# Optimization experiments

Hardware: AMD Instinct MI355X
Metric: run time of the kernel (lower is better)

The kernel has to match this reference:

```python
import jax, jax.numpy as jnp
import numpy as np
from jax.ops import segment_sum, segment_max

N_NODES = 100000
N_EDGES = 1600000
IN_CH = 128
HIDDEN = 128
OUT_CH = 64
HEADS1 = 8


def _lin_params(key, din, dout, scale):
    kw, kb = jax.random.split(key)
    W = jax.random.normal(kw, (din, dout), jnp.float32) * scale
    b = jax.random.normal(kb, (dout,), jnp.float32) * 0.01
    return W, b


def setup_inputs() -> dict:
    key = jax.random.key(0)
    ks = jax.random.split(key, 10)
    x = jax.random.normal(ks[0], (N_NODES, IN_CH), jnp.float32)
    edge_index = jax.random.randint(ks[1], (2, N_EDGES), 0, N_NODES, jnp.int32)
    s1 = 1.0 / np.sqrt(IN_CH)
    Wq1, bq1 = _lin_params(ks[2], IN_CH, HIDDEN, s1)
    Wk1, bk1 = _lin_params(ks[3], IN_CH, HIDDEN, s1)
    Wv1, bv1 = _lin_params(ks[4], IN_CH, HIDDEN, s1)
    Ws1, bs1 = _lin_params(ks[5], IN_CH, HIDDEN, s1)
    s2 = 1.0 / np.sqrt(HIDDEN)
    Wq2, bq2 = _lin_params(ks[6], HIDDEN, OUT_CH, s2)
    Wk2, bk2 = _lin_params(ks[7], HIDDEN, OUT_CH, s2)
    Wv2, bv2 = _lin_params(ks[8], HIDDEN, OUT_CH, s2)
    Ws2, bs2 = _lin_params(ks[9], HIDDEN, OUT_CH, s2)
    return dict(x=x, edge_index=edge_index,
                Wq1=Wq1, bq1=bq1, Wk1=Wk1, bk1=bk1, Wv1=Wv1, bv1=bv1, Ws1=Ws1, bs1=bs1,
                Wq2=Wq2, bq2=bq2, Wk2=Wk2, bk2=bk2, Wv2=Wv2, bv2=bv2, Ws2=Ws2, bs2=bs2)


def transformer_conv(x, src, dst, Wq, bq, Wk, bk, Wv, bv, Ws, bs, heads, concat):
    # x: [N, Din]; src/dst: [E]; per-head dim C = Dout_total // heads
    N = x.shape[0]
    C = Wq.shape[1] // heads
    q = (x @ Wq + bq).reshape(N, heads, C)
    k = (x @ Wk + bk).reshape(N, heads, C)
    v = (x @ Wv + bv).reshape(N, heads, C)
    # edge-wise gather + dot-product attention logits: [E, H]
    alpha = jnp.einsum('ehc,ehc->eh', q[dst], k[src]) / np.sqrt(C)
    # softmax over incoming edges of each dst node (stable via segment max)
    m = segment_max(alpha, dst, num_segments=N)  # [N, H]
    ex = jnp.exp(alpha - jax.lax.stop_gradient(m)[dst])
    denom = segment_sum(ex, dst, num_segments=N)  # [N, H]
    alpha_n = ex / denom[dst]  # [E, H]
    out = segment_sum(v[src] * alpha_n[:, :, None], dst, num_segments=N)  # [N, H, C]
    skip = x @ Ws + bs  # root weight (PyG root_weight=True)
    if concat:
        out = out.reshape(N, heads * C) + skip
    else:
        out = out.mean(axis=1) + skip
    return out


def reference(x, edge_index,
              Wq1, bq1, Wk1, bk1, Wv1, bv1, Ws1, bs1,
              Wq2, bq2, Wk2, bk2, Wv2, bv2, Ws2, bs2):
    src, dst = edge_index[0], edge_index[1]
    h = transformer_conv(x, src, dst, Wq1, bq1, Wk1, bk1, Wv1, bv1, Ws1, bs1,
                         heads=HEADS1, concat=True)
    h = jax.nn.relu(h)  # dropout is identity in eval mode
    out = transformer_conv(h, src, dst, Wq2, bq2, Wk2, bk2, Wv2, bv2, Ws2, bs2,
                           heads=1, concat=False)
    return out
```

## Files before the change

### kernel.cpp

```cpp
#include <hip/hip_runtime.h>
#include <math.h>

#define NN 100000
#define NPAD 100096
#define NE 1600000
#define NB 391
#define BKSH 8
#define EPB 6250
#define CSTAGE 5120
#define NDEG 64
#define DTOT (NDEG * NB)

typedef __attribute__((ext_vector_type(8))) short bf16x8;
typedef __attribute__((ext_vector_type(4))) float f32x4;

__device__ __forceinline__ unsigned short f2bf(float x) {
  unsigned int u = __float_as_uint(x);
  u += 0x7fffu + ((u >> 16) & 1u);
  return (unsigned short)(u >> 16);
}
__device__ __forceinline__ float bf2f(unsigned short b) {
  return __uint_as_float(((unsigned int)b) << 16);
}
__device__ __forceinline__ void unpack8(uint4 u, float* f) {
  f[0] = __uint_as_float(u.x << 16); f[1] = __uint_as_float(u.x & 0xffff0000u);
  f[2] = __uint_as_float(u.y << 16); f[3] = __uint_as_float(u.y & 0xffff0000u);
  f[4] = __uint_as_float(u.z << 16); f[5] = __uint_as_float(u.z & 0xffff0000u);
  f[6] = __uint_as_float(u.w << 16); f[7] = __uint_as_float(u.w & 0xffff0000u);
}
__device__ __forceinline__ void split8(const float* f, bf16x8& h8, bf16x8& l8) {
  union { bf16x8 v; unsigned short s[8]; } H, L;
  #pragma unroll
  for (int j = 0; j < 8; ++j) {
    const unsigned short hh = f2bf(f[j]);
    H.s[j] = hh;
    L.s[j] = f2bf(f[j] - bf2f(hh));
  }
  h8 = H.v; l8 = L.v;
}
__device__ __forceinline__ void gl_lds16(const void* g, void* lds) {
  __builtin_amdgcn_global_load_lds(
      (const __attribute__((address_space(1))) unsigned int*)g,
      (__attribute__((address_space(3))) unsigned int*)lds, 16, 0, 0);
}

#define PIPE_WAIT4  asm volatile("s_waitcnt vmcnt(4)\n\ts_barrier" ::: "memory")
#define PIPE_WAIT36 asm volatile("s_waitcnt vmcnt(36)\n\ts_barrier" ::: "memory")
#define PIPE_WAIT0  asm volatile("s_waitcnt vmcnt(0)\n\ts_barrier" ::: "memory")
#define PIPE_BAR    asm volatile("s_barrier" ::: "memory")
#define PIPE_FENCE  asm volatile("" ::: "memory")

__global__ __launch_bounds__(256)
void bktcnt_k(const int* __restrict__ dst, int* __restrict__ gcnt) {
  __shared__ int cnt[NB];
  for (int i = threadIdx.x; i < NB; i += 256) cnt[i] = 0;
  __syncthreads();
  const int e0 = blockIdx.x * EPB;
  for (int e = e0 + threadIdx.x; e < e0 + EPB; e += 256)
    atomicAdd(&cnt[dst[e] >> BKSH], 1);
  __syncthreads();
  for (int i = threadIdx.x; i < NB; i += 256)
    if (cnt[i]) atomicAdd(&gcnt[i], cnt[i]);
}

__global__ void bktscan_k(const int* __restrict__ gcnt, int* __restrict__ base,
                          int* __restrict__ cursor) {
  __shared__ int sh[512];
  const int t = threadIdx.x;
  const int v = (t < NB) ? gcnt[t] : 0;
  sh[t] = v;
  __syncthreads();
  #pragma unroll
  for (int off = 1; off < 512; off <<= 1) {
    int nv = (t >= off) ? sh[t - off] : 0;
    __syncthreads();
    sh[t] += nv;
    __syncthreads();
  }
  const int excl = sh[t] - v;
  if (t < NB) { base[t] = excl; cursor[t] = excl; }
  if (t == NB - 1) base[NB] = excl + v;
}

__global__ __launch_bounds__(256)
void bktscat_k(const int* __restrict__ src, const int* __restrict__ dst,
               int* __restrict__ cursor, unsigned int* __restrict__ pairs) {
  __shared__ int cnt[NB];
  __shared__ int bbase[NB];
  for (int i = threadIdx.x; i < NB; i += 256) cnt[i] = 0;
  __syncthreads();
  const int e0 = blockIdx.x * EPB;
  for (int e = e0 + threadIdx.x; e < e0 + EPB; e += 256)
    atomicAdd(&cnt[dst[e] >> BKSH], 1);
  __syncthreads();
  for (int i = threadIdx.x; i < NB; i += 256) {
    bbase[i] = cnt[i] ? atomicAdd(&cursor[i], cnt[i]) : 0;
    cnt[i] = 0;
  }
  __syncthreads();
  for (int e = e0 + threadIdx.x; e < e0 + EPB; e += 256) {
    const int d = dst[e];
    const int b = d >> BKSH;
    const int loc = atomicAdd(&cnt[b], 1);
    pairs[bbase[b] + loc] = ((unsigned)src[e] << BKSH) | (unsigned)(d & 255);
  }
}

__global__ __launch_bounds__(256)
void bktcsr_k(const unsigned int* __restrict__ pairs, const int* __restrict__ base,
              int* __restrict__ rowp, int* __restrict__ cidx) {
  __shared__ int cnt[256];
  __shared__ int sums[256];
  __shared__ int stage[CSTAGE];
  const int b = blockIdx.x, t = threadIdx.x;
  const int p0 = base[b], p1 = base[b + 1], bs = p1 - p0;
  const int n0 = b << BKSH;
  const int nloc = (NN - n0 < 256) ? (NN - n0) : 256;
  cnt[t] = 0;
  __syncthreads();
  for (int i = p0 + t; i < p1; i += 256)
    atomicAdd(&cnt[pairs[i] & 255], 1);
  __syncthreads();
  const int v = cnt[t];
  sums[t] = v;
  __syncthreads();
  #pragma unroll
  for (int off = 1; off < 256; off <<= 1) {
    int nv = (t >= off) ? sums[t - off] : 0;
    __syncthreads();
    sums[t] += nv;
    __syncthreads();
  }
  const int myexcl = sums[t] - v;
  if (t < nloc) rowp[n0 + t] = p0 + myexcl;
  if (b == 0 && t == 0) rowp[NN] = base[NB];
  __syncthreads();
  cnt[t] = myexcl;
  __syncthreads();
  if (bs <= CSTAGE) {
    for (int i = p0 + t; i < p1; i += 256) {
      const unsigned pk = pairs[i];
      const int loc = atomicAdd(&cnt[pk & 255], 1);
      stage[loc] = (int)(pk >> BKSH);
    }
    __syncthreads();
    for (int i = t; i < bs; i += 256) cidx[p0 + i] = stage[i];
  } else {
    for (int i = p0 + t; i < p1; i += 256) {
      const unsigned pk = pairs[i];
      const int loc = atomicAdd(&cnt[pk & 255], 1);
      cidx[p0 + loc] = (int)(pk >> BKSH);
    }
  }
}

__global__ __launch_bounds__(256)
void dcnt_k(const int* __restrict__ rowp, int* __restrict__ gdcnt) {
  __shared__ int h[NDEG];
  const int t = threadIdx.x, b = blockIdx.x;
  if (t < NDEG) h[t] = 0;
  __syncthreads();
  const int n = b * 256 + t;
  if (n < NN) {
    int d = rowp[n + 1] - rowp[n];
    if (d > NDEG - 1) d = NDEG - 1;
    atomicAdd(&h[d], 1);
  }
  __syncthreads();
  if (t < NDEG) gdcnt[t * NB + b] = h[t];
}

__global__ __launch_bounds__(1024)
void dscan2_k(int* __restrict__ g) {
  __shared__ int part[1024];
  const int t = threadIdx.x;
  constexpr int PER = (DTOT + 1023) / 1024;
  int vals[PER];
  const int base = t * PER;
  int sum = 0;
  #pragma unroll
  for (int i = 0; i < PER; ++i) {
    const int idx = base + i;
    const int v = (idx < DTOT) ? g[idx] : 0;
    vals[i] = sum;
    sum += v;
  }
  part[t] = sum;
  __syncthreads();
  #pragma unroll
  for (int off = 1; off < 1024; off <<= 1) {
    int nv = (t >= off) ? part[t - off] : 0;
    __syncthreads();
    part[t] += nv;
    __syncthreads();
  }
  const int excl = part[t] - sum;
  #pragma unroll
  for (int i = 0; i < PER; ++i) {
    const int idx = base + i;
    if (idx < DTOT) g[idx] = excl + vals[i];
  }
}

__global__ __launch_bounds__(256)
void dperm2_k(const int* __restrict__ rowp, const int* __restrict__ gdcnt,
              int* __restrict__ perm) {
  __shared__ int lcur[NDEG];
  const int t = threadIdx.x, b = blockIdx.x;
  if (t < NDEG) lcur[t] = 0;
  __syncthreads();
  const int n = b * 256 + t;
  if (n < NN) {
    int d = rowp[n + 1] - rowp[n];
    if (d > NDEG - 1) d = NDEG - 1;
    const int r = atomicAdd(&lcur[d], 1);
    perm[NN - 1 - (gdcnt[d * NB + b] + r)] = n;
  }
}

struct WConv { const float* src; unsigned short* hi; unsigned short* lo; int dout; };
struct WConv8 { WConv m[8]; };

__global__ void wconv_k(WConv8 a) {
  const WConv w = a.m[blockIdx.x];
  const int n = 128 * w.dout;
  for (int i = threadIdx.x; i < n; i += blockDim.x) {
    const int c = i >> 7, kk = i & 127;
    const float x = w.src[(size_t)kk * w.dout + c];
    const unsigned short h = f2bf(x);
    w.hi[i] = h;
    w.lo[i] = f2bf(x - bf2f(h));
  }
}

struct GMat { const unsigned short* wh; const unsigned short* wl;
              const float* bias; float* outf; unsigned short* outb; };
struct GArgs { GMat m[4]; };

template <int DOUT, bool PRESPLIT>
__global__ __launch_bounds__(256, 3)
void gemm4_mfma(const float* __restrict__ X,
                const unsigned short* __restrict__ Xh,
                const unsigned short* __restrict__ Xl,
                int nrows, GArgs ga) {
  constexpr int NCG = DOUT / 64;
  constexpr int NS = 4 * NCG * 2;
  __shared__ __align__(16) unsigned short Bs[2][8192];
  const int t = threadIdx.x;
  const int w = t >> 6, l = t & 63;
  const int lr = l & 15, lg = l >> 4;
  const int row0 = blockIdx.x * 128;

  float bias_r[4][NCG][4];
  #pragma unroll
  for (int m = 0; m < 4; ++m)
    #pragma unroll
    for (int cg = 0; cg < NCG; ++cg)
      #pragma unroll
      for (int nf = 0; nf < 4; ++nf)
        bias_r[m][cg][nf] = ga.m[m].bias[cg * 64 + nf * 16 + lr];

  bf16x8 ah[2][4], al[2][4];
  #pragma unroll
  for (int rf = 0; rf < 2; ++rf) {
    const int r = row0 + w * 32 + rf * 16 + lr;
    if constexpr (!PRESPLIT) {
      const bool ok = r < nrows;
      const float* xp = &X[(size_t)r * 128];
      #pragma unroll
      for (int ks = 0; ks < 4; ++ks) {
        float f[8];
        if (ok) {
          *(float4*)&f[0] = *(const float4*)&xp[ks * 32 + lg * 8];
          *(float4*)&f[4] = *(const float4*)&xp[ks * 32 + lg * 8 + 4];
        } else {
          #pragma unroll
          for (int j = 0; j < 8; ++j) f[j] = 0.f;
        }
        split8(f, ah[rf][ks], al[rf][ks]);
      }
    } else {
      #pragma unroll
      for (int ks = 0; ks < 4; ++ks) {
        ah[rf][ks] = *(const bf16x8*)&Xh[(size_t)r * 128 + ks * 32 + lg * 8];
        al[rf][ks] = *(const bf16x8*)&Xl[(size_t)r * 128 + ks * 32 + lg * 8];
      }
    }
  }
  PIPE_FENCE;

  auto stage = [&](int buf, int s) {
    const int m = s / (NCG * 2);
    const int rem = s - m * (NCG * 2);
    const int cg = rem >> 1, pl = rem & 1;
    const char* gb = (const char*)((pl ? ga.m[m].wl : ga.m[m].wh) + cg * 64 * 128);
    char* lb = (char*)&Bs[buf][0];
    #pragma unroll
    for (int i = 0; i < 4; ++i) {
      const int seg = (w * 4 + i) << 10;
      const int o = seg + l * 16;
      const int osw = o ^ (((o >> 8) & 7) << 4);
      gl_lds16(gb + osw, lb + seg);
    }
  };

  f32x4 acc[4][2];
  stage(0, 0);
  int cur = 0;
  const int sw = (lr & 7) << 4;
  #pragma unroll
  for (int s = 0; s < NS; ++s) {
    if (s + 1 < NS) stage(cur ^ 1, s + 1);
    if (s == NS - 1)                { PIPE_WAIT0; }
    else if (s >= 2 && !(s & 1))    { PIPE_WAIT36; }
    else                            { PIPE_WAIT4;  }
    const int m = s / (NCG * 2);
    const int rem = s - m * (NCG * 2);
    const int cg = rem >> 1, pl = rem & 1;
    const char* lbase = (const char*)&Bs[cur][0];
    if (pl == 0) {
      #pragma unroll
      for (int nf = 0; nf < 4; ++nf) {
        const char* lp = lbase + nf * 4096 + lr * 256;
        bf16x8 bq[4];
        #pragma unroll
        for (int ks = 0; ks < 4; ++ks)
          bq[ks] = *(const bf16x8*)(lp + (((ks * 64 + lg * 16) ^ sw)));
        f32x4 a0 = {0.f, 0.f, 0.f, 0.f}, a1 = a0;
        #pragma unroll
        for (int ks = 0; ks < 4; ++ks) {
          a0 = __builtin_amdgcn_mfma_f32_16x16x32_bf16(ah[0][ks], bq[ks], a0, 0, 0, 0);
          a1 = __builtin_amdgcn_mfma_f32_16x16x32_bf16(ah[1][ks], bq[ks], a1, 0, 0, 0);
        }
        #pragma unroll
        for (int ks = 0; ks < 4; ++ks) {
          a0 = __builtin_amdgcn_mfma_f32_16x16x32_bf16(al[0][ks], bq[ks], a0, 0, 0, 0);
          a1 = __builtin_amdgcn_mfma_f32_16x16x32_bf16(al[1][ks], bq[ks], a1, 0, 0, 0);
        }
        acc[nf][0] = a0; acc[nf][1] = a1;
      }
    } else {
      const GMat gm = ga.m[m];
      #pragma unroll
      for (int nf = 0; nf < 4; ++nf) {
        const char* lp = lbase + nf * 4096 + lr * 256;
        bf16x8 bq[4];
        #pragma unroll
        for (int ks = 0; ks < 4; ++ks)
          bq[ks] = *(const bf16x8*)(lp + (((ks * 64 + lg * 16) ^ sw)));
        f32x4 a0 = acc[nf][0], a1 = acc[nf][1];
        #pragma unroll
        for (int ks = 0; ks < 4; ++ks) {
          a0 = __builtin_amdgcn_mfma_f32_16x16x32_bf16(ah[0][ks], bq[ks], a0, 0, 0, 0);
          a1 = __builtin_amdgcn_mfma_f32_16x16x32_bf16(ah[1][ks], bq[ks], a1, 0, 0, 0);
        }
        const int col = cg * 64 + nf * 16 + lr;
        const float bb = bias_r[m][cg][nf];
        #pragma unroll
        for (int j = 0; j < 4; ++j) {
          const int r0 = row0 + w * 32 + lg * 4 + j;
          const int r1 = r0 + 16;
          if (gm.outb) {
            gm.outb[(size_t)r0 * DOUT + col] = f2bf(a0[j] + bb);
            gm.outb[(size_t)r1 * DOUT + col] = f2bf(a1[j] + bb);
          } else {
            gm.outf[(size_t)r0 * DOUT + col] = a0[j] + bb;
            gm.outf[(size_t)r1 * DOUT + col] = a1[j] + bb;
          }
        }
      }
    }
    if (s + 1 < NS) PIPE_BAR;
    cur ^= 1;
  }
}

__global__ __launch_bounds__(256)
void attn1_k(const unsigned short* __restrict__ q, const unsigned short* __restrict__ k,
             const unsigned short* __restrict__ v, const float* __restrict__ skip,
             const int* __restrict__ rowp, const int* __restrict__ cidx,
             const int* __restrict__ perm,
             unsigned short* __restrict__ hhi, unsigned short* __restrict__ hlo) {
  const int idx = blockIdx.x * 32 + (threadIdx.x >> 3);
  if (idx >= NN) return;
  const int node = perm[idx];
  const int cb = (threadIdx.x & 7) * 16;
  float qv[16];
  {
    uint4 q0 = *(const uint4*)&q[(size_t)node * 128 + cb];
    uint4 q1 = *(const uint4*)&q[(size_t)node * 128 + cb + 8];
    unpack8(q0, qv); unpack8(q1, qv + 8);
    #pragma unroll
    for (int c = 0; c < 16; ++c) qv[c] *= 0.25f;
  }
  float s = 0.f, acc[16];
  #pragma unroll
  for (int c = 0; c < 16; ++c) acc[c] = 0.f;
  const int e0 = rowp[node], e1 = rowp[node + 1];
  int e = e0;
  for (; e + 3 < e1; e += 4) {
    int sidx[4];
    #pragma unroll
    for (int j = 0; j < 4; ++j) sidx[j] = cidx[e + j];
    uint4 K[4][2], V[4][2];
    #pragma unroll
    for (int j = 0; j < 4; ++j) {
      const size_t o = (size_t)sidx[j] * 128 + cb;
      K[j][0] = *(const uint4*)&k[o];
      K[j][1] = *(const uint4*)&k[o + 8];
      V[j][0] = *(const uint4*)&v[o];
      V[j][1] = *(const uint4*)&v[o + 8];
    }
    float pr[4];
    #pragma unroll
    for (int j = 0; j < 4; ++j) {
      float kv[16];
      unpack8(K[j][0], kv); unpack8(K[j][1], kv + 8);
      float d = 0.f;
      #pragma unroll
      for (int c = 0; c < 16; ++c) d = fmaf(qv[c], kv[c], d);
      pr[j] = __expf(d);
      s += pr[j];
    }
    #pragma unroll
    for (int j = 0; j < 4; ++j) {
      float vv[16];
      unpack8(V[j][0], vv); unpack8(V[j][1], vv + 8);
      #pragma unroll
      for (int c = 0; c < 16; ++c) acc[c] = fmaf(pr[j], vv[c], acc[c]);
    }
  }
  for (; e < e1; ++e) {
    const int sa = cidx[e];
    uint4 k0 = *(const uint4*)&k[(size_t)sa * 128 + cb];
    uint4 k1 = *(const uint4*)&k[(size_t)sa * 128 + cb + 8];
    uint4 v0 = *(const uint4*)&v[(size_t)sa * 128 + cb];
    uint4 v1 = *(const uint4*)&v[(size_t)sa * 128 + cb + 8];
    float kv[16]; unpack8(k0, kv); unpack8(k1, kv + 8);
    float d = 0.f;
    #pragma unroll
    for (int c = 0; c < 16; ++c) d = fmaf(qv[c], kv[c], d);
    const float p = __expf(d);
    s += p;
    float vv[16]; unpack8(v0, vv); unpack8(v1, vv + 8);
    #pragma unroll
    for (int c = 0; c < 16; ++c) acc[c] = fmaf(p, vv[c], acc[c]);
  }
  const float inv = (e1 > e0) ? 1.f / s : 0.f;
  float sk[16];
  {
    const float* sp = &skip[(size_t)node * 128 + cb];
    *(float4*)&sk[0]  = *(const float4*)&sp[0];
    *(float4*)&sk[4]  = *(const float4*)&sp[4];
    *(float4*)&sk[8]  = *(const float4*)&sp[8];
    *(float4*)&sk[12] = *(const float4*)&sp[12];
  }
  unsigned int hw[8], lw[8];
  #pragma unroll
  for (int c2 = 0; c2 < 8; ++c2) {
    const float oa = fmaxf(fmaf(acc[2 * c2], inv, sk[2 * c2]), 0.f);
    const float ob = fmaxf(fmaf(acc[2 * c2 + 1], inv, sk[2 * c2 + 1]), 0.f);
    const unsigned short ha = f2bf(oa), hb = f2bf(ob);
    hw[c2] = (unsigned)ha | ((unsigned)hb << 16);
    lw[c2] = (unsigned)f2bf(oa - bf2f(ha)) | ((unsigned)f2bf(ob - bf2f(hb)) << 16);
  }
  uint4* HH = (uint4*)&hhi[(size_t)node * 128 + cb];
  uint4* LL = (uint4*)&hlo[(size_t)node * 128 + cb];
  HH[0] = make_uint4(hw[0], hw[1], hw[2], hw[3]);
  HH[1] = make_uint4(hw[4], hw[5], hw[6], hw[7]);
  LL[0] = make_uint4(lw[0], lw[1], lw[2], lw[3]);
  LL[1] = make_uint4(lw[4], lw[5], lw[6], lw[7]);
}

__global__ __launch_bounds__(256)
void attn2_k(const unsigned short* __restrict__ q, const unsigned short* __restrict__ k,
             const unsigned short* __restrict__ v, const float* __restrict__ skip,
             const int* __restrict__ rowp, const int* __restrict__ cidx,
             const int* __restrict__ perm, float* __restrict__ out) {
  const int idx = blockIdx.x * 32 + (threadIdx.x >> 3);
  if (idx >= NN) return;
  const int node = perm[idx];
  const int cb = (threadIdx.x & 7) * 8;
  float qv[8];
  {
    uint4 q0 = *(const uint4*)&q[(size_t)node * 64 + cb];
    unpack8(q0, qv);
    #pragma unroll
    for (int c = 0; c < 8; ++c) qv[c] *= 0.125f;
  }
  float s = 0.f, acc[8];
  #pragma unroll
  for (int c = 0; c < 8; ++c) acc[c] = 0.f;
  const int e0 = rowp[node], e1 = rowp[node + 1];
  int e = e0;
  for (; e + 3 < e1; e += 4) {
    int sidx[4];
    #pragma unroll
    for (int j = 0; j < 4; ++j) sidx[j] = cidx[e + j];
    uint4 K[4], V[4];
    #pragma unroll
    for (int j = 0; j < 4; ++j) {
      const size_t o = (size_t)sidx[j] * 64 + cb;
      K[j] = *(const uint4*)&k[o];
      V[j] = *(const uint4*)&v[o];
    }
    float dd[4];
    #pragma unroll
    for (int j = 0; j < 4; ++j) {
      float kv[8]; unpack8(K[j], kv);
      float d = 0.f;
      #pragma unroll
      for (int c = 0; c < 8; ++c) d = fmaf(qv[c], kv[c], d);
      dd[j] = d;
    }
    #pragma unroll
    for (int j = 0; j < 4; ++j) {
      dd[j] += __shfl_xor(dd[j], 1);
      dd[j] += __shfl_xor(dd[j], 2);
      dd[j] += __shfl_xor(dd[j], 4);
    }
    #pragma unroll
    for (int j = 0; j < 4; ++j) {
      const float p = __expf(dd[j]);
      s += p;
      float vv[8]; unpack8(V[j], vv);
      #pragma unroll
      for (int c = 0; c < 8; ++c) acc[c] = fmaf(p, vv[c], acc[c]);
    }
  }
  for (; e < e1; ++e) {
    const int sa = cidx[e];
    uint4 kk = *(const uint4*)&k[(size_t)sa * 64 + cb];
    uint4 vv4 = *(const uint4*)&v[(size_t)sa * 64 + cb];
    float kv[8]; unpack8(kk, kv);
    float d = 0.f;
    #pragma unroll
    for (int c = 0; c < 8; ++c) d = fmaf(qv[c], kv[c], d);
    d += __shfl_xor(d, 1);
    d += __shfl_xor(d, 2);
    d += __shfl_xor(d, 4);
    const float p = __expf(d);
    s += p;
    float vv[8]; unpack8(vv4, vv);
    #pragma unroll
    for (int c = 0; c < 8; ++c) acc[c] = fmaf(p, vv[c], acc[c]);
  }
  const float inv = (e1 > e0) ? 1.f / s : 0.f;
  const float* sp = &skip[(size_t)node * 64 + cb];
  float4 o0, o1;
  o0.x = fmaf(acc[0], inv, sp[0]); o0.y = fmaf(acc[1], inv, sp[1]);
  o0.z = fmaf(acc[2], inv, sp[2]); o0.w = fmaf(acc[3], inv, sp[3]);
  o1.x = fmaf(acc[4], inv, sp[4]); o1.y = fmaf(acc[5], inv, sp[5]);
  o1.z = fmaf(acc[6], inv, sp[6]); o1.w = fmaf(acc[7], inv, sp[7]);
  *(float4*)&out[(size_t)node * 64 + cb] = o0;
  *(float4*)&out[(size_t)node * 64 + cb + 4] = o1;
}

extern "C" void kernel_launch(void* const* d_in, const int* in_sizes, int n_in,
                              void* d_out, int out_size, void* d_ws, size_t ws_size,
                              hipStream_t stream) {
  const float* x = (const float*)d_in[0];
  const int* ei = (const int*)d_in[1];
  const int* esrc = ei;
  const int* edst = ei + NE;
  const float* Wf[8] = {(const float*)d_in[2],  (const float*)d_in[4],
                        (const float*)d_in[6],  (const float*)d_in[8],
                        (const float*)d_in[10], (const float*)d_in[12],
                        (const float*)d_in[14], (const float*)d_in[16]};
  const float* Bf[8] = {(const float*)d_in[3],  (const float*)d_in[5],
                        (const float*)d_in[7],  (const float*)d_in[9],
                        (const float*)d_in[11], (const float*)d_in[13],
                        (const float*)d_in[15], (const float*)d_in[17]};
  float* out = (float*)d_out;

  char* p = (char*)d_ws;
  auto alloc = [&](size_t b) { char* r = p; p += (b + 255) & ~(size_t)255; return r; };
  unsigned short* q1 = (unsigned short*)alloc((size_t)NPAD * 128 * 2);
  unsigned short* k1 = (unsigned short*)alloc((size_t)NPAD * 128 * 2);
  unsigned short* v1 = (unsigned short*)alloc((size_t)NPAD * 128 * 2);
  float*          sk1 = (float*)alloc((size_t)NPAD * 128 * 4);
  unsigned short* hh = (unsigned short*)alloc((size_t)NPAD * 128 * 2);
  unsigned short* hl = (unsigned short*)alloc((size_t)NPAD * 128 * 2);
  unsigned short* q2 = (unsigned short*)alloc((size_t)NPAD * 64 * 2);
  unsigned short* k2 = (unsigned short*)alloc((size_t)NPAD * 64 * 2);
  unsigned short* v2 = (unsigned short*)alloc((size_t)NPAD * 64 * 2);
  float*          sk2 = (float*)alloc((size_t)NPAD * 64 * 4);
  unsigned short* wh[8];
  unsigned short* wl[8];
  for (int i = 0; i < 8; ++i) {
    const int dout = (i < 4) ? 128 : 64;
    wh[i] = (unsigned short*)alloc((size_t)128 * dout * 2);
    wl[i] = (unsigned short*)alloc((size_t)128 * dout * 2);
  }
  int* rowp = (int*)alloc((size_t)(NN + 1) * 4);
  int* cidx = (int*)alloc((size_t)NE * 4);
  int* gcnt = (int*)alloc((size_t)NB * 4);
  int* base = (int*)alloc((size_t)(NB + 1) * 4);
  int* cursor = (int*)alloc((size_t)NB * 4);
  int* gdcnt = (int*)alloc((size_t)DTOT * 4);
  int* perm = (int*)alloc((size_t)NN * 4);
  unsigned int* pairs = (unsigned int*)hh;

  WConv8 wc;
  for (int i = 0; i < 8; ++i) wc.m[i] = {Wf[i], wh[i], wl[i], (i < 4) ? 128 : 64};
  wconv_k<<<8, 1024, 0, stream>>>(wc);

  hipMemsetAsync(gcnt, 0, NB * sizeof(int), stream);
  bktcnt_k<<<256, 256, 0, stream>>>(edst, gcnt);
  bktscan_k<<<1, 512, 0, stream>>>(gcnt, base, cursor);
  bktscat_k<<<256, 256, 0, stream>>>(esrc, edst, cursor, pairs);
  bktcsr_k<<<NB, 256, 0, stream>>>(pairs, base, rowp, cidx);

  dcnt_k<<<NB, 256, 0, stream>>>(rowp, gdcnt);
  dscan2_k<<<1, 1024, 0, stream>>>(gdcnt);
  dperm2_k<<<NB, 256, 0, stream>>>(rowp, gdcnt, perm);

  GArgs g1;
  g1.m[0] = {wh[0], wl[0], Bf[0], nullptr, q1};
  g1.m[1] = {wh[1], wl[1], Bf[1], nullptr, k1};
  g1.m[2] = {wh[2], wl[2], Bf[2], nullptr, v1};
  g1.m[3] = {wh[3], wl[3], Bf[3], sk1, nullptr};
  gemm4_mfma<128, false><<<NPAD / 128, 256, 0, stream>>>(x, nullptr, nullptr, NN, g1);
  attn1_k<<<(NN + 31) / 32, 256, 0, stream>>>(q1, k1, v1, sk1, rowp, cidx, perm, hh, hl);

  GArgs g2;
  g2.m[0] = {wh[4], wl[4], Bf[4], nullptr, q2};
  g2.m[1] = {wh[5], wl[5], Bf[5], nullptr, k2};
  g2.m[2] = {wh[6], wl[6], Bf[6], nullptr, v2};
  g2.m[3] = {wh[7], wl[7], Bf[7], sk2, nullptr};
  gemm4_mfma<64, true><<<NPAD / 128, 256, 0, stream>>>(nullptr, hh, hl, NN, g2);
  attn2_k<<<(NN + 31) / 32, 256, 0, stream>>>(q2, k2, v2, sk2, rowp, cidx, perm, out);
}
```

Baseline: 433.7 us.

## Split GEMM across two matrix groups, store skip in bf16, fuse degree histogram

The degree histogram moves into the CSR build kernel, which removes the separate dcnt launch and its rowp reread. The projection GEMM now uses a 2-D grid where each block computes two of the four matrices, with bias staged in shared memory. This frees registers, allowing occupancy 4, and doubles the block count. Skip outputs are stored as bf16 instead of fp32, halving that traffic, at some precision loss on the skip term. The cost is that every block now loads the X rows twice, once per grid-y slice.

Result: slower. 496.9 us (+14.6%).

```diff
diff --git a/kernel.cpp b/kernel.cpp
--- a/kernel.cpp
+++ b/kernel.cpp
@@ -108,21 +108,28 @@
 
 __global__ __launch_bounds__(256)
 void bktcsr_k(const unsigned int* __restrict__ pairs, const int* __restrict__ base,
-              int* __restrict__ rowp, int* __restrict__ cidx) {
+              int* __restrict__ rowp, int* __restrict__ cidx,
+              int* __restrict__ gdcnt) {
   __shared__ int cnt[256];
   __shared__ int sums[256];
+  __shared__ int hdeg[NDEG];
   __shared__ int stage[CSTAGE];
   const int b = blockIdx.x, t = threadIdx.x;
   const int p0 = base[b], p1 = base[b + 1], bs = p1 - p0;
   const int n0 = b << BKSH;
   const int nloc = (NN - n0 < 256) ? (NN - n0) : 256;
   cnt[t] = 0;
+  if (t < NDEG) hdeg[t] = 0;
   __syncthreads();
   for (int i = p0 + t; i < p1; i += 256)
     atomicAdd(&cnt[pairs[i] & 255], 1);
   __syncthreads();
   const int v = cnt[t];
   sums[t] = v;
+  if (t < nloc) {
+    int d = (v > NDEG - 1) ? NDEG - 1 : v;
+    atomicAdd(&hdeg[d], 1);
+  }
   __syncthreads();
   #pragma unroll
   for (int off = 1; off < 256; off <<= 1) {
@@ -134,6 +141,7 @@
   const int myexcl = sums[t] - v;
   if (t < nloc) rowp[n0 + t] = p0 + myexcl;
   if (b == 0 && t == 0) rowp[NN] = base[NB];
+  if (t < NDEG) gdcnt[t * NB + b] = hdeg[t];
   __syncthreads();
   cnt[t] = myexcl;
   __syncthreads();
@@ -152,22 +160,6 @@
       cidx[p0 + loc] = (int)(pk >> BKSH);
     }
   }
-}
-
-__global__ __launch_bounds__(256)
-void dcnt_k(const int* __restrict__ rowp, int* __restrict__ gdcnt) {
-  __shared__ int h[NDEG];
-  const int t = threadIdx.x, b = blockIdx.x;
-  if (t < NDEG) h[t] = 0;
-  __syncthreads();
-  const int n = b * 256 + t;
-  if (n < NN) {
-    int d = rowp[n + 1] - rowp[n];
-    if (d > NDEG - 1) d = NDEG - 1;
-    atomicAdd(&h[d], 1);
-  }
-  __syncthreads();
-  if (t < NDEG) gdcnt[t * NB + b] = h[t];
 }
 
 __global__ __launch_bounds__(1024)
@@ -234,31 +226,28 @@
 }
 
 struct GMat { const unsigned short* wh; const unsigned short* wl;
-              const float* bias; float* outf; unsigned short* outb; };
+              const float* bias; unsigned short* outb; };
 struct GArgs { GMat m[4]; };
 
 template <int DOUT, bool PRESPLIT>
-__global__ __launch_bounds__(256, 3)
+__global__ __launch_bounds__(256, 4)
 void gemm4_mfma(const float* __restrict__ X,
                 const unsigned short* __restrict__ Xh,
                 const unsigned short* __restrict__ Xl,
                 int nrows, GArgs ga) {
   constexpr int NCG = DOUT / 64;
-  constexpr int NS = 4 * NCG * 2;
+  constexpr int NS = 2 * NCG * 2;
   __shared__ __align__(16) unsigned short Bs[2][8192];
+  __shared__ float BiasS[2][DOUT];
+  const int mb = blockIdx.y * 2;
   const int t = threadIdx.x;
   const int w = t >> 6, l = t & 63;
   const int lr = l & 15, lg = l >> 4;
   const int row0 = blockIdx.x * 128;
 
-  float bias_r[4][NCG][4];
-  #pragma unroll
-  for (int m = 0; m < 4; ++m)
-    #pragma unroll
-    for (int cg = 0; cg < NCG; ++cg)
-      #pragma unroll
-      for (int nf = 0; nf < 4; ++nf)
-        bias_r[m][cg][nf] = ga.m[m].bias[cg * 64 + nf * 16 + lr];
+  for (int i = t; i < 2 * DOUT; i += 256)
+    BiasS[i / DOUT][i % DOUT] = ga.m[mb + i / DOUT].bias[i % DOUT];
+  __syncthreads();
 
   bf16x8 ah[2][4], al[2][4];
   #pragma unroll
@@ -290,10 +279,11 @@
   PIPE_FENCE;
 
   auto stage = [&](int buf, int s) {
-    const int m = s / (NCG * 2);
-    const int rem = s - m * (NCG * 2);
+    const int ml = s / (NCG * 2);
+    const int rem = s - ml * (NCG * 2);
     const int cg = rem >> 1, pl = rem & 1;
-    const char* gb = (const char*)((pl ? ga.m[m].wl : ga.m[m].wh) + cg * 64 * 128);
+    const GMat& gm = ga.m[mb + ml];
+    const char* gb = (const char*)((pl ? gm.wl : gm.wh) + cg * 64 * 128);
     char* lb = (char*)&Bs[buf][0];
     #pragma unroll
     for (int i = 0; i < 4; ++i) {
@@ -311,11 +301,11 @@
   #pragma unroll
   for (int s = 0; s < NS; ++s) {
     if (s + 1 < NS) stage(cur ^ 1, s + 1);
-    if (s == NS - 1)                { PIPE_WAIT0; }
-    else if (s >= 2 && !(s & 1))    { PIPE_WAIT36; }
-    else                            { PIPE_WAIT4;  }
-    const int m = s / (NCG * 2);
-    const int rem = s - m * (NCG * 2);
+    if (s == NS - 1)              { PIPE_WAIT0; }
+    else if (s >= 2 && !(s & 1))  { PIPE_WAIT36; }
+    else                          { PIPE_WAIT4;  }
+    const int ml = s / (NCG * 2);
+    const int rem = s - ml * (NCG * 2);
     const int cg = rem >> 1, pl = rem & 1;
     const char* lbase = (const char*)&Bs[cur][0];
     if (pl == 0) {
@@ -340,7 +330,7 @@
         acc[nf][0] = a0; acc[nf][1] = a1;
       }
     } else {
-      const GMat gm = ga.m[m];
+      const GMat gm = ga.m[mb + ml];
       #pragma unroll
       for (int nf = 0; nf < 4; ++nf) {
         const char* lp = lbase + nf * 4096 + lr * 256;
@@ -355,18 +345,13 @@
           a1 = __builtin_amdgcn_mfma_f32_16x16x32_bf16(ah[1][ks], bq[ks], a1, 0, 0, 0);
         }
         const int col = cg * 64 + nf * 16 + lr;
-        const float bb = bias_r[m][cg][nf];
+        const float bb = BiasS[ml][col];
         #pragma unroll
         for (int j = 0; j < 4; ++j) {
           const int r0 = row0 + w * 32 + lg * 4 + j;
           const int r1 = r0 + 16;
-          if (gm.outb) {
-            gm.outb[(size_t)r0 * DOUT + col] = f2bf(a0[j] + bb);
-            gm.outb[(size_t)r1 * DOUT + col] = f2bf(a1[j] + bb);
-          } else {
-            gm.outf[(size_t)r0 * DOUT + col] = a0[j] + bb;
-            gm.outf[(size_t)r1 * DOUT + col] = a1[j] + bb;
-          }
+          gm.outb[(size_t)r0 * DOUT + col] = f2bf(a0[j] + bb);
+          gm.outb[(size_t)r1 * DOUT + col] = f2bf(a1[j] + bb);
         }
       }
     }
@@ -377,7 +362,7 @@
 
 __global__ __launch_bounds__(256)
 void attn1_k(const unsigned short* __restrict__ q, const unsigned short* __restrict__ k,
-             const unsigned short* __restrict__ v, const float* __restrict__ skip,
+             const unsigned short* __restrict__ v, const unsigned short* __restrict__ skip,
              const int* __restrict__ rowp, const int* __restrict__ cidx,
              const int* __restrict__ perm,
              unsigned short* __restrict__ hhi, unsigned short* __restrict__ hlo) {
@@ -449,11 +434,10 @@
   const float inv = (e1 > e0) ? 1.f / s : 0.f;
   float sk[16];
   {
-    const float* sp = &skip[(size_t)node * 128 + cb];
-    *(float4*)&sk[0]  = *(const float4*)&sp[0];
-    *(float4*)&sk[4]  = *(const float4*)&sp[4];
-    *(float4*)&sk[8]  = *(const float4*)&sp[8];
-    *(float4*)&sk[12] = *(const float4*)&sp[12];
+    const unsigned short* sp = &skip[(size_t)node * 128 + cb];
+    uint4 s0v = *(const uint4*)&sp[0];
+    uint4 s1v = *(const uint4*)&sp[8];
+    unpack8(s0v, sk); unpack8(s1v, sk + 8);
   }
   unsigned int hw[8], lw[8];
   #pragma unroll
@@ -474,7 +458,7 @@
 
 __global__ __launch_bounds__(256)
 void attn2_k(const unsigned short* __restrict__ q, const unsigned short* __restrict__ k,
-             const unsigned short* __restrict__ v, const float* __restrict__ skip,
+             const unsigned short* __restrict__ v, const unsigned short* __restrict__ skip,
              const int* __restrict__ rowp, const int* __restrict__ cidx,
              const int* __restrict__ perm, float* __restrict__ out) {
   const int idx = blockIdx.x * 32 + (threadIdx.x >> 3);
@@ -546,12 +530,17 @@
     for (int c = 0; c < 8; ++c) acc[c] = fmaf(p, vv[c], acc[c]);
   }
   const float inv = (e1 > e0) ? 1.f / s : 0.f;
-  const float* sp = &skip[(size_t)node * 64 + cb];
+  float sk[8];
+  {
+    const unsigned short* sp = &skip[(size_t)node * 64 + cb];
+    uint4 sv = *(const uint4*)&sp[0];
+    unpack8(sv, sk);
+  }
   float4 o0, o1;
-  o0.x = fmaf(acc[0], inv, sp[0]); o0.y = fmaf(acc[1], inv, sp[1]);
-  o0.z = fmaf(acc[2], inv, sp[2]); o0.w = fmaf(acc[3], inv, sp[3]);
-  o1.x = fmaf(acc[4], inv, sp[4]); o1.y = fmaf(acc[5], inv, sp[5]);
-  o1.z = fmaf(acc[6], inv, sp[6]); o1.w = fmaf(acc[7], inv, sp[7]);
+  o0.x = fmaf(acc[0], inv, sk[0]); o0.y = fmaf(acc[1], inv, sk[1]);
+  o0.z = fmaf(acc[2], inv, sk[2]); o0.w = fmaf(acc[3], inv, sk[3]);
+  o1.x = fmaf(acc[4], inv, sk[4]); o1.y = fmaf(acc[5], inv, sk[5]);
+  o1.z = fmaf(acc[6], inv, sk[6]); o1.w = fmaf(acc[7], inv, sk[7]);
   *(float4*)&out[(size_t)node * 64 + cb] = o0;
   *(float4*)&out[(size_t)node * 64 + cb + 4] = o1;
 }
@@ -578,13 +567,13 @@
   unsigned short* q1 = (unsigned short*)alloc((size_t)NPAD * 128 * 2);
   unsigned short* k1 = (unsigned short*)alloc((size_t)NPAD * 128 * 2);
   unsigned short* v1 = (unsigned short*)alloc((size_t)NPAD * 128 * 2);
-  float*          sk1 = (float*)alloc((size_t)NPAD * 128 * 4);
+  unsigned short* sk1 = (unsigned short*)alloc((size_t)NPAD * 128 * 2);
   unsigned short* hh = (unsigned short*)alloc((size_t)NPAD * 128 * 2);
   unsigned short* hl = (unsigned short*)alloc((size_t)NPAD * 128 * 2);
   unsigned short* q2 = (unsigned short*)alloc((size_t)NPAD * 64 * 2);
   unsigned short* k2 = (unsigned short*)alloc((size_t)NPAD * 64 * 2);
   unsigned short* v2 = (unsigned short*)alloc((size_t)NPAD * 64 * 2);
-  float*          sk2 = (float*)alloc((size_t)NPAD * 64 * 4);
+  unsigned short* sk2 = (unsigned short*)alloc((size_t)NPAD * 64 * 2);
   unsigned short* wh[8];
   unsigned short* wl[8];
   for (int i = 0; i < 8; ++i) {
@@ -609,25 +598,26 @@
   bktcnt_k<<<256, 256, 0, stream>>>(edst, gcnt);
   bktscan_k<<<1, 512, 0, stream>>>(gcnt, base, cursor);
   bktscat_k<<<256, 256, 0, stream>>>(esrc, edst, cursor, pairs);
-  bktcsr_k<<<NB, 256, 0, stream>>>(pairs, base, rowp, cidx);
-
-  dcnt_k<<<NB, 256, 0, stream>>>(rowp, gdcnt);
+  bktcsr_k<<<NB, 256, 0, stream>>>(pairs, base, rowp, cidx, gdcnt);
+
   dscan2_k<<<1, 1024, 0, stream>>>(gdcnt);
   dperm2_k<<<NB, 256, 0, stream>>>(rowp, gdcnt, perm);
 
   GArgs g1;
-  g1.m[0] = {wh[0], wl[0], Bf[0], nullptr, q1};
-  g1.m[1] = {wh[1], wl[1], Bf[1], nullptr, k1};
-  g1.m[2] = {wh[2], wl[2], Bf[2], nullptr, v1};
-  g1.m[3] = {wh[3], wl[3], Bf[3], sk1, nullptr};
-  gemm4_mfma<128, false><<<NPAD / 128, 256, 0, stream>>>(x, nullptr, nullptr, NN, g1);
+  g1.m[0] = {wh[0], wl[0], Bf[0], q1};
+  g1.m[1] = {wh[1], wl[1], Bf[1], k1};
+  g1.m[2] = {wh[2], wl[2], Bf[2], v1};
+  g1.m[3] = {wh[3], wl[3], Bf[3], sk1};
+  gemm4_mfma<128, false><<<dim3(NPAD / 128, 2), 256, 0, stream>>>(
+      x, nullptr, nullptr, NN, g1);
   attn1_k<<<(NN + 31) / 32, 256, 0, stream>>>(q1, k1, v1, sk1, rowp, cidx, perm, hh, hl);
 
   GArgs g2;
-  g2.m[0] = {wh[4], wl[4], Bf[4], nullptr, q2};
-  g2.m[1] = {wh[5], wl[5], Bf[5], nullptr, k2};
-  g2.m[2] = {wh[6], wl[6], Bf[6], nullptr, v2};
-  g2.m[3] = {wh[7], wl[7], Bf[7], sk2, nullptr};
-  gemm4_mfma<64, true><<<NPAD / 128, 256, 0, stream>>>(nullptr, hh, hl, NN, g2);
+  g2.m[0] = {wh[4], wl[4], Bf[4], q2};
+  g2.m[1] = {wh[5], wl[5], Bf[5], k2};
+  g2.m[2] = {wh[6], wl[6], Bf[6], v2};
+  g2.m[3] = {wh[7], wl[7], Bf[7], sk2};
+  gemm4_mfma<64, true><<<dim3(NPAD / 128, 2), 256, 0, stream>>>(
+      nullptr, hh, hl, NN, g2);
   attn2_k<<<(NN + 31) / 32, 256, 0, stream>>>(q2, k2, v2, sk2, rowp, cidx, perm, out);
 }
```
